# Kernel tuning notes

Hardware: AMD Instinct MI355X
Metric: run time of the kernel (lower is better)

## Reference

```python
import jax, jax.numpy as jnp
import numpy as np

N_NODES = 50000
N_EDGES = 800000
X_DIM = 64
STATE_DIM = 64
IN_DIM = X_DIM + STATE_DIM
OUT_DIM = 64
N_HEADS = 4
HEAD_DIM = OUT_DIM // N_HEADS
NEG_SLOPE = 0.2


def setup_inputs() -> dict:
    key = jax.random.key(0)
    ks = jax.random.split(key, 7)
    x = jax.random.normal(ks[0], (N_NODES, X_DIM), dtype=jnp.float32)
    state = jax.random.normal(ks[1], (N_NODES, STATE_DIM), dtype=jnp.float32)
    edge_index = jax.random.randint(ks[2], (2, N_EDGES), 0, N_NODES, dtype=jnp.int64)
    edge_weight = jax.random.uniform(ks[3], (N_EDGES,), dtype=jnp.float32)
    # xavier-uniform-like scales
    w_scale = float(np.sqrt(2.0 / (IN_DIM + OUT_DIM)))
    a_scale = float(np.sqrt(2.0 / (N_HEADS + HEAD_DIM)))
    W = jax.random.normal(ks[4], (OUT_DIM, IN_DIM), dtype=jnp.float32) * w_scale
    attn_src = jax.random.normal(ks[5], (N_HEADS, HEAD_DIM), dtype=jnp.float32) * a_scale
    attn_dst = jax.random.normal(ks[6], (N_HEADS, HEAD_DIM), dtype=jnp.float32) * a_scale
    return {"x": x, "state": state, "edge_index": edge_index, "edge_weight": edge_weight,
            "W": W, "attn_src": attn_src, "attn_dst": attn_dst}


def reference(x, state, edge_index, edge_weight, W, attn_src, attn_dst):
    # edge_weight is ignored by design (pure attention behavior)
    del edge_weight
    N = x.shape[0]
    H, D = attn_src.shape
    # linear_in (no bias): [N, IN_DIM] @ [IN_DIM, OUT_DIM]
    h_flat = jnp.concatenate([x, state], axis=-1) @ W.T          # [N, OUT_DIM]
    h = h_flat.reshape(N, H, D)                                   # [N, H, D]
    src = edge_index[0]
    dst = edge_index[1]
    # per-node attention scores, then gather per-edge (same math as gathering h first)
    s_src = jnp.einsum('nhd,hd->nh', h, attn_src)                 # [N, H]
    s_dst = jnp.einsum('nhd,hd->nh', h, attn_dst)                 # [N, H]
    logits = s_src[src] + s_dst[dst]                              # [E, H]
    logits = jnp.where(logits >= 0, logits, NEG_SLOPE * logits)   # leaky_relu
    # segment softmax over incoming edges of each dst node (stable, two-pass)
    max_by_dst = jax.ops.segment_max(logits, dst, num_segments=N) # [N, H]
    exp_shifted = jnp.exp(logits - max_by_dst[dst])               # [E, H]
    denom = jax.ops.segment_sum(exp_shifted, dst, num_segments=N) # [N, H]
    alpha = exp_shifted / (denom[dst] + 1e-12)                    # [E, H]
    # weighted message aggregation
    msg = h[src] * alpha[:, :, None]                              # [E, H, D]
    out_flat = jax.ops.segment_sum(msg.reshape(msg.shape[0], H * D), dst, num_segments=N)
    out_flat = out_flat + h_flat                                  # residual (shapes always match)
    out_flat = jax.nn.elu(out_flat)                               # activation
    return out_flat
```

## Files before the change

### kernel.cpp

```cpp
#include <hip/hip_runtime.h>
#include <hip/hip_bf16.h>

#define N_NODES 50000
#define N_EDGES 800000
#define NBK 196
#define BCAP 40
#define CAP  4864

typedef __attribute__((ext_vector_type(8))) short bf16x8;
typedef __attribute__((ext_vector_type(4))) float f32x4;

__device__ __forceinline__ unsigned short f2bu(float f) {
    __hip_bfloat16 hb = __float2bfloat16(f);
    return *(unsigned short*)&hb;
}
__device__ __forceinline__ unsigned pk2(float a, float b) {
    return (unsigned)f2bu(a) | ((unsigned)f2bu(b) << 16);
}

__global__ void __launch_bounds__(256, 4)
k1_mfma(const float* __restrict__ x, const float* __restrict__ state,
        const float* __restrict__ W, const float* __restrict__ a_src,
        const float* __restrict__ a_dst,
        float* __restrict__ hf32, float* __restrict__ s_src4,
        float* __restrict__ s_dst4, int* __restrict__ gcur) {
    __shared__ unsigned short alds[64 * 136];
    __shared__ unsigned short wlds[64 * 136];
    int tid = threadIdx.x;
    int nb = blockIdx.x * 64;

    if (blockIdx.x == 0 && tid < NBK) gcur[tid] = 0;

    const float4* x4  = (const float4*)x;
    const float4* st4 = (const float4*)state;
    const float4* W4  = (const float4*)W;
    for (int idx = tid; idx < 2048; idx += 256) {
        int row = idx >> 5, qc = idx & 31;
        int n = nb + row;
        float4 v = make_float4(0.f, 0.f, 0.f, 0.f);
        if (n < N_NODES)
            v = (qc < 16) ? x4[(long)n * 16 + qc] : st4[(long)n * 16 + (qc - 16)];
        unsigned* ap = (unsigned*)&alds[row * 136 + qc * 4];
        ap[0] = pk2(v.x, v.y);
        ap[1] = pk2(v.z, v.w);
        float4 wv = W4[idx];
        unsigned* wp = (unsigned*)&wlds[row * 136 + qc * 4];
        wp[0] = pk2(wv.x, wv.y);
        wp[1] = pk2(wv.z, wv.w);
    }
    __syncthreads();

    int lane = tid & 63;
    int w = tid >> 6;
    int lrow = lane & 15, lq = lane >> 4;

    f32x4 acc[4];
#pragma unroll
    for (int c = 0; c < 4; ++c) acc[c] = (f32x4){0.f, 0.f, 0.f, 0.f};

#pragma unroll
    for (int kc = 0; kc < 4; ++kc) {
        bf16x8 af = *(const bf16x8*)&alds[(w * 16 + lrow) * 136 + kc * 32 + lq * 8];
#pragma unroll
        for (int c = 0; c < 4; ++c) {
            bf16x8 bf = *(const bf16x8*)&wlds[(c * 16 + lrow) * 136 + kc * 32 + lq * 8];
            acc[c] = __builtin_amdgcn_mfma_f32_16x16x32_bf16(af, bf, acc[c], 0, 0, 0);
        }
    }
    __syncthreads();

    float* hst = (float*)alds;
#pragma unroll
    for (int r = 0; r < 4; ++r) {
        int nl = w * 16 + lq * 4 + r;
#pragma unroll
        for (int c = 0; c < 4; ++c)
            hst[nl * 68 + c * 16 + lrow] = acc[c][r];
    }
    __syncthreads();

    int node = tid >> 2, chunk = tid & 3;
    int n = nb + node;
    if (n < N_NODES) {
        const float* hp = &hst[node * 68 + chunk * 16];
        float hv[16];
        float vs = 0.f, vd = 0.f;
#pragma unroll
        for (int i = 0; i < 16; ++i) {
            hv[i] = hp[i];
            vs = fmaf(hv[i], a_src[chunk * 16 + i], vs);
            vd = fmaf(hv[i], a_dst[chunk * 16 + i], vd);
        }
        float* dst = hf32 + (long)n * 64 + chunk * 16;
        *(float4*)(dst + 0)  = make_float4(hv[0],  hv[1],  hv[2],  hv[3]);
        *(float4*)(dst + 4)  = make_float4(hv[4],  hv[5],  hv[6],  hv[7]);
        *(float4*)(dst + 8)  = make_float4(hv[8],  hv[9],  hv[10], hv[11]);
        *(float4*)(dst + 12) = make_float4(hv[12], hv[13], hv[14], hv[15]);
        s_src4[(long)nb * 4 + tid] = vs;
        s_dst4[(long)nb * 4 + tid] = vd;
    }
}

__global__ void __launch_bounds__(256)
k_bin(const int* __restrict__ ei, int* __restrict__ gcur, int* __restrict__ recs) {
    __shared__ int cnt[NBK];
    __shared__ int stage[NBK][BCAP];
    int tid = threadIdx.x;
    for (int i = tid; i < NBK; i += 256) cnt[i] = 0;
    __syncthreads();
    int e0 = blockIdx.x * 4096;
#pragma unroll
    for (int k = 0; k < 4; ++k) {
        int e = e0 + k * 1024 + tid * 4;
        if (e < N_EDGES) {
            int4 sv = *(const int4*)(ei + e);
            int4 dv = *(const int4*)(ei + N_EDGES + e);
            int ss[4] = {sv.x, sv.y, sv.z, sv.w};
            int dd[4] = {dv.x, dv.y, dv.z, dv.w};
#pragma unroll
            for (int j = 0; j < 4; ++j) {
                int b = dd[j] >> 8;
                int rec = ss[j] | ((dd[j] & 255) << 16);
                int p = atomicAdd(&cnt[b], 1);
                if (p < BCAP) stage[b][p] = rec;
                else {
                    int g = atomicAdd(&gcur[b], 1);
                    recs[b * CAP + g] = rec;
                }
            }
        }
    }
    __syncthreads();
    for (int b = tid; b < NBK; b += 256) {
        int nb = min(cnt[b], BCAP);
        if (nb > 0) {
            int g = atomicAdd(&gcur[b], nb);
            int d0 = b * CAP + g;
            for (int i = 0; i < nb; ++i) recs[d0 + i] = stage[b][i];
        }
    }
}

__global__ void __launch_bounds__(256)
k_sort(const int* __restrict__ recs, const int* __restrict__ gcur,
       int* __restrict__ recs2, int* __restrict__ off, int* __restrict__ deg) {
    __shared__ int cnt[256];
    __shared__ int pos[256];
    __shared__ int wsum[4];
    int tid = threadIdx.x, b = blockIdx.x;
    cnt[tid] = 0;
    __syncthreads();
    int base = b * CAP, cntb = gcur[b];
    for (int i = tid; i < cntb; i += 256)
        atomicAdd(&cnt[(recs[base + i] >> 16) & 255], 1);
    __syncthreads();
    int lane = tid & 63, wid = tid >> 6;
    int v = cnt[tid], inc = v;
#pragma unroll
    for (int s = 1; s < 64; s <<= 1) {
        int t = __shfl_up(inc, s);
        if (lane >= s) inc += t;
    }
    if (lane == 63) wsum[wid] = inc;
    __syncthreads();
    if (tid == 0) {
        int s = 0;
#pragma unroll
        for (int w = 0; w < 4; ++w) { int t = wsum[w]; wsum[w] = s; s += t; }
    }
    __syncthreads();
    int excl = wsum[wid] + inc - v;
    pos[tid] = excl;
    int n = b * 256 + tid;
    if (n < N_NODES) { off[n] = base + excl; deg[n] = v; }
    __syncthreads();
    for (int i = tid; i < cntb; i += 256) {
        int r = recs[base + i];
        int p = atomicAdd(&pos[(r >> 16) & 255], 1);
        recs2[base + p] = r & 0xFFFF;
    }
}

__global__ void k_agg(const int* __restrict__ off, const int* __restrict__ deg,
                      const int* __restrict__ csr, const float* __restrict__ s_src4,
                      const float* __restrict__ s_dst4,
                      const float* __restrict__ hf32, float* __restrict__ out) {
    int wave = threadIdx.x >> 6, lane = threadIdx.x & 63;
    int n = blockIdx.x * 4 + wave;
    if (n >= N_NODES) return;
    int q = lane >> 3, d = lane & 7, hh = d >> 1;
    int b = off[n], nE = deg[n];
    float sdh = s_dst4[(long)n * 4 + hh];

    float den = 0.f;
    float a0 = 0, a1 = 0, a2 = 0, a3 = 0, a4 = 0, a5 = 0, a6 = 0, a7 = 0;
    for (int c = 0; c < nE; c += 64) {
        int jn = min(64, nE - c);
        int svl = (lane < jn) ? csr[b + c + lane] : 0;
        for (int j = 0; j < jn; j += 16) {
            int j0 = j + q, j1 = j + 8 + q;
            float m0 = (j0 < jn) ? 1.f : 0.f;
            float m1 = (j1 < jn) ? 1.f : 0.f;
            int s0 = __shfl(svl, j0);
            int s1 = __shfl(svl, j1);
            float l0 = s_src4[s0 * 4 + hh];
            float l1 = s_src4[s1 * 4 + hh];
            const float4* p0 = (const float4*)(hf32 + (long)s0 * 64 + 8 * d);
            const float4* p1 = (const float4*)(hf32 + (long)s1 * 64 + 8 * d);
            float4 A0 = p0[0], A1 = p0[1];
            float4 B0 = p1[0], B1 = p1[1];
            l0 += sdh; l1 += sdh;
            float e0 = m0 * __expf(fmaxf(l0, 0.2f * l0));
            float e1 = m1 * __expf(fmaxf(l1, 0.2f * l1));
            den += e0 + e1;
            a0 = fmaf(e0, A0.x, a0); a1 = fmaf(e0, A0.y, a1);
            a2 = fmaf(e0, A0.z, a2); a3 = fmaf(e0, A0.w, a3);
            a4 = fmaf(e0, A1.x, a4); a5 = fmaf(e0, A1.y, a5);
            a6 = fmaf(e0, A1.z, a6); a7 = fmaf(e0, A1.w, a7);
            a0 = fmaf(e1, B0.x, a0); a1 = fmaf(e1, B0.y, a1);
            a2 = fmaf(e1, B0.z, a2); a3 = fmaf(e1, B0.w, a3);
            a4 = fmaf(e1, B1.x, a4); a5 = fmaf(e1, B1.y, a5);
            a6 = fmaf(e1, B1.z, a6); a7 = fmaf(e1, B1.w, a7);
        }
    }
#pragma unroll
    for (int o2 = 8; o2 < 64; o2 <<= 1) {
        den += __shfl_xor(den, o2);
        a0 += __shfl_xor(a0, o2);
        a1 += __shfl_xor(a1, o2);
        a2 += __shfl_xor(a2, o2);
        a3 += __shfl_xor(a3, o2);
        a4 += __shfl_xor(a4, o2);
        a5 += __shfl_xor(a5, o2);
        a6 += __shfl_xor(a6, o2);
        a7 += __shfl_xor(a7, o2);
    }

    if (q == 0) {
        const float4* hrp = (const float4*)(hf32 + (long)n * 64 + 8 * d);
        float4 r0 = hrp[0], r1 = hrp[1];
        float inv = 1.0f / (den + 1e-12f);
        float o0 = a0 * inv + r0.x, o1 = a1 * inv + r0.y;
        float o2 = a2 * inv + r0.z, o3 = a3 * inv + r0.w;
        float o4 = a4 * inv + r1.x, o5 = a5 * inv + r1.y;
        float o6 = a6 * inv + r1.z, o7 = a7 * inv + r1.w;
        o0 = (o0 > 0.f) ? o0 : __expf(o0) - 1.f;
        o1 = (o1 > 0.f) ? o1 : __expf(o1) - 1.f;
        o2 = (o2 > 0.f) ? o2 : __expf(o2) - 1.f;
        o3 = (o3 > 0.f) ? o3 : __expf(o3) - 1.f;
        o4 = (o4 > 0.f) ? o4 : __expf(o4) - 1.f;
        o5 = (o5 > 0.f) ? o5 : __expf(o5) - 1.f;
        o6 = (o6 > 0.f) ? o6 : __expf(o6) - 1.f;
        o7 = (o7 > 0.f) ? o7 : __expf(o7) - 1.f;
        float* op = &out[(long)n * 64 + 8 * d];
        *(float4*)(op + 0) = make_float4(o0, o1, o2, o3);
        *(float4*)(op + 4) = make_float4(o4, o5, o6, o7);
    }
}

extern "C" void kernel_launch(void* const* d_in, const int* in_sizes, int n_in,
                              void* d_out, int out_size, void* d_ws, size_t ws_size,
                              hipStream_t stream) {
    const float* x      = (const float*)d_in[0];
    const float* state  = (const float*)d_in[1];
    const int*   ei     = (const int*)d_in[2];
    const float* W      = (const float*)d_in[4];
    const float* a_src  = (const float*)d_in[5];
    const float* a_dst  = (const float*)d_in[6];

    float* out = (float*)d_out;

    float* hf32   = (float*)d_ws;
    float* s_src4 = hf32 + (long)N_NODES * 64;
    float* s_dst4 = s_src4 + (long)N_NODES * 4;
    int*   gcur   = (int*)(s_dst4 + (long)N_NODES * 4);
    int*   off    = gcur + 256;
    int*   deg    = off + N_NODES;
    int*   recs   = deg + N_NODES;
    int*   recs2  = recs + (long)NBK * CAP;

    k1_mfma<<<782, 256, 0, stream>>>(x, state, W, a_src, a_dst,
                                     hf32, s_src4, s_dst4, gcur);
    k_bin<<<196, 256, 0, stream>>>(ei, gcur, recs);
    k_sort<<<NBK, 256, 0, stream>>>(recs, gcur, recs2, off, deg);
    k_agg<<<(N_NODES + 3) / 4, 256, 0, stream>>>(off, deg, recs2, s_src4, s_dst4, hf32, out);
}
```

Baseline: 73.22 us.

## Store node features in bf16 and double rows per block in projection kernel

The projection kernel now writes h as packed bf16 instead of fp32, and the aggregation kernel gathers and unpacks bf16 rows, which halves the bytes moved per edge gather and for the residual. The projection kernel also processes 128 nodes per block, with two MFMA row tiles per wave, and launches half as many blocks. This reduces gather memory traffic at the cost of bf16 rounding in both the message values and the residual term.

```diff
diff --git a/kernel.cpp b/kernel.cpp
--- a/kernel.cpp
+++ b/kernel.cpp
@@ -10,6 +10,8 @@
 typedef __attribute__((ext_vector_type(8))) short bf16x8;
 typedef __attribute__((ext_vector_type(4))) float f32x4;
 
+__device__ __forceinline__ float blo(unsigned u) { return __uint_as_float(u << 16); }
+__device__ __forceinline__ float bhi(unsigned u) { return __uint_as_float(u & 0xffff0000u); }
 __device__ __forceinline__ unsigned short f2bu(float f) {
     __hip_bfloat16 hb = __float2bfloat16(f);
     return *(unsigned short*)&hb;
@@ -18,23 +20,23 @@
     return (unsigned)f2bu(a) | ((unsigned)f2bu(b) << 16);
 }
 
-__global__ void __launch_bounds__(256, 4)
+__global__ void __launch_bounds__(256, 3)
 k1_mfma(const float* __restrict__ x, const float* __restrict__ state,
         const float* __restrict__ W, const float* __restrict__ a_src,
         const float* __restrict__ a_dst,
-        float* __restrict__ hf32, float* __restrict__ s_src4,
+        unsigned short* __restrict__ hf2, float* __restrict__ s_src4,
         float* __restrict__ s_dst4, int* __restrict__ gcur) {
-    __shared__ unsigned short alds[64 * 136];
+    __shared__ unsigned short alds[128 * 136];
     __shared__ unsigned short wlds[64 * 136];
     int tid = threadIdx.x;
-    int nb = blockIdx.x * 64;
+    int nb = blockIdx.x * 128;
 
     if (blockIdx.x == 0 && tid < NBK) gcur[tid] = 0;
 
     const float4* x4  = (const float4*)x;
     const float4* st4 = (const float4*)state;
     const float4* W4  = (const float4*)W;
-    for (int idx = tid; idx < 2048; idx += 256) {
+    for (int idx = tid; idx < 4096; idx += 256) {
         int row = idx >> 5, qc = idx & 31;
         int n = nb + row;
         float4 v = make_float4(0.f, 0.f, 0.f, 0.f);
@@ -43,6 +45,9 @@
         unsigned* ap = (unsigned*)&alds[row * 136 + qc * 4];
         ap[0] = pk2(v.x, v.y);
         ap[1] = pk2(v.z, v.w);
+    }
+    for (int idx = tid; idx < 2048; idx += 256) {
+        int row = idx >> 5, qc = idx & 31;
         float4 wv = W4[idx];
         unsigned* wp = (unsigned*)&wlds[row * 136 + qc * 4];
         wp[0] = pk2(wv.x, wv.y);
@@ -54,50 +59,60 @@
     int w = tid >> 6;
     int lrow = lane & 15, lq = lane >> 4;
 
-    f32x4 acc[4];
-#pragma unroll
-    for (int c = 0; c < 4; ++c) acc[c] = (f32x4){0.f, 0.f, 0.f, 0.f};
+    f32x4 acc[2][4];
+#pragma unroll
+    for (int rt = 0; rt < 2; ++rt)
+#pragma unroll
+        for (int c = 0; c < 4; ++c) acc[rt][c] = (f32x4){0.f, 0.f, 0.f, 0.f};
 
 #pragma unroll
     for (int kc = 0; kc < 4; ++kc) {
-        bf16x8 af = *(const bf16x8*)&alds[(w * 16 + lrow) * 136 + kc * 32 + lq * 8];
+        bf16x8 af0 = *(const bf16x8*)&alds[(w * 32 + lrow) * 136 + kc * 32 + lq * 8];
+        bf16x8 af1 = *(const bf16x8*)&alds[(w * 32 + 16 + lrow) * 136 + kc * 32 + lq * 8];
 #pragma unroll
         for (int c = 0; c < 4; ++c) {
             bf16x8 bf = *(const bf16x8*)&wlds[(c * 16 + lrow) * 136 + kc * 32 + lq * 8];
-            acc[c] = __builtin_amdgcn_mfma_f32_16x16x32_bf16(af, bf, acc[c], 0, 0, 0);
+            acc[0][c] = __builtin_amdgcn_mfma_f32_16x16x32_bf16(af0, bf, acc[0][c], 0, 0, 0);
+            acc[1][c] = __builtin_amdgcn_mfma_f32_16x16x32_bf16(af1, bf, acc[1][c], 0, 0, 0);
         }
     }
     __syncthreads();
 
     float* hst = (float*)alds;
 #pragma unroll
-    for (int r = 0; r < 4; ++r) {
-        int nl = w * 16 + lq * 4 + r;
-#pragma unroll
-        for (int c = 0; c < 4; ++c)
-            hst[nl * 68 + c * 16 + lrow] = acc[c][r];
-    }
-    __syncthreads();
-
-    int node = tid >> 2, chunk = tid & 3;
-    int n = nb + node;
-    if (n < N_NODES) {
-        const float* hp = &hst[node * 68 + chunk * 16];
-        float hv[16];
-        float vs = 0.f, vd = 0.f;
-#pragma unroll
-        for (int i = 0; i < 16; ++i) {
-            hv[i] = hp[i];
-            vs = fmaf(hv[i], a_src[chunk * 16 + i], vs);
-            vd = fmaf(hv[i], a_dst[chunk * 16 + i], vd);
-        }
-        float* dst = hf32 + (long)n * 64 + chunk * 16;
-        *(float4*)(dst + 0)  = make_float4(hv[0],  hv[1],  hv[2],  hv[3]);
-        *(float4*)(dst + 4)  = make_float4(hv[4],  hv[5],  hv[6],  hv[7]);
-        *(float4*)(dst + 8)  = make_float4(hv[8],  hv[9],  hv[10], hv[11]);
-        *(float4*)(dst + 12) = make_float4(hv[12], hv[13], hv[14], hv[15]);
-        s_src4[(long)nb * 4 + tid] = vs;
-        s_dst4[(long)nb * 4 + tid] = vd;
+    for (int rt = 0; rt < 2; ++rt)
+#pragma unroll
+        for (int r = 0; r < 4; ++r) {
+            int nl = w * 32 + rt * 16 + lq * 4 + r;
+#pragma unroll
+            for (int c = 0; c < 4; ++c)
+                hst[nl * 68 + c * 16 + lrow] = acc[rt][c][r];
+        }
+    __syncthreads();
+
+#pragma unroll
+    for (int g = 0; g < 2; ++g) {
+        int node = (tid >> 2) + g * 64, chunk = tid & 3;
+        int n = nb + node;
+        if (n < N_NODES) {
+            const float* hp = &hst[node * 68 + chunk * 16];
+            float hv[16];
+            float vs = 0.f, vd = 0.f;
+#pragma unroll
+            for (int i = 0; i < 16; ++i) {
+                hv[i] = hp[i];
+                vs = fmaf(hv[i], a_src[chunk * 16 + i], vs);
+                vd = fmaf(hv[i], a_dst[chunk * 16 + i], vd);
+            }
+            unsigned pk[8];
+#pragma unroll
+            for (int j = 0; j < 8; ++j) pk[j] = pk2(hv[2 * j], hv[2 * j + 1]);
+            uint4* dst = (uint4*)(hf2 + (long)n * 64 + chunk * 16);
+            dst[0] = make_uint4(pk[0], pk[1], pk[2], pk[3]);
+            dst[1] = make_uint4(pk[4], pk[5], pk[6], pk[7]);
+            s_src4[(long)n * 4 + chunk] = vs;
+            s_dst4[(long)n * 4 + chunk] = vd;
+        }
     }
 }
 
@@ -184,7 +199,7 @@
 __global__ void k_agg(const int* __restrict__ off, const int* __restrict__ deg,
                       const int* __restrict__ csr, const float* __restrict__ s_src4,
                       const float* __restrict__ s_dst4,
-                      const float* __restrict__ hf32, float* __restrict__ out) {
+                      const unsigned short* __restrict__ h2, float* __restrict__ out) {
     int wave = threadIdx.x >> 6, lane = threadIdx.x & 63;
     int n = blockIdx.x * 4 + wave;
     if (n >= N_NODES) return;
@@ -205,22 +220,20 @@
             int s1 = __shfl(svl, j1);
             float l0 = s_src4[s0 * 4 + hh];
             float l1 = s_src4[s1 * 4 + hh];
-            const float4* p0 = (const float4*)(hf32 + (long)s0 * 64 + 8 * d);
-            const float4* p1 = (const float4*)(hf32 + (long)s1 * 64 + 8 * d);
-            float4 A0 = p0[0], A1 = p0[1];
-            float4 B0 = p1[0], B1 = p1[1];
+            uint4 A = *(const uint4*)(h2 + (long)s0 * 64 + 8 * d);
+            uint4 B = *(const uint4*)(h2 + (long)s1 * 64 + 8 * d);
             l0 += sdh; l1 += sdh;
             float e0 = m0 * __expf(fmaxf(l0, 0.2f * l0));
             float e1 = m1 * __expf(fmaxf(l1, 0.2f * l1));
             den += e0 + e1;
-            a0 = fmaf(e0, A0.x, a0); a1 = fmaf(e0, A0.y, a1);
-            a2 = fmaf(e0, A0.z, a2); a3 = fmaf(e0, A0.w, a3);
-            a4 = fmaf(e0, A1.x, a4); a5 = fmaf(e0, A1.y, a5);
-            a6 = fmaf(e0, A1.z, a6); a7 = fmaf(e0, A1.w, a7);
-            a0 = fmaf(e1, B0.x, a0); a1 = fmaf(e1, B0.y, a1);
-            a2 = fmaf(e1, B0.z, a2); a3 = fmaf(e1, B0.w, a3);
-            a4 = fmaf(e1, B1.x, a4); a5 = fmaf(e1, B1.y, a5);
-            a6 = fmaf(e1, B1.z, a6); a7 = fmaf(e1, B1.w, a7);
+            a0 = fmaf(e0, blo(A.x), a0); a1 = fmaf(e0, bhi(A.x), a1);
+            a2 = fmaf(e0, blo(A.y), a2); a3 = fmaf(e0, bhi(A.y), a3);
+            a4 = fmaf(e0, blo(A.z), a4); a5 = fmaf(e0, bhi(A.z), a5);
+            a6 = fmaf(e0, blo(A.w), a6); a7 = fmaf(e0, bhi(A.w), a7);
+            a0 = fmaf(e1, blo(B.x), a0); a1 = fmaf(e1, bhi(B.x), a1);
+            a2 = fmaf(e1, blo(B.y), a2); a3 = fmaf(e1, bhi(B.y), a3);
+            a4 = fmaf(e1, blo(B.z), a4); a5 = fmaf(e1, bhi(B.z), a5);
+            a6 = fmaf(e1, blo(B.w), a6); a7 = fmaf(e1, bhi(B.w), a7);
         }
     }
 #pragma unroll
@@ -237,13 +250,12 @@
     }
 
     if (q == 0) {
-        const float4* hrp = (const float4*)(hf32 + (long)n * 64 + 8 * d);
-        float4 r0 = hrp[0], r1 = hrp[1];
+        uint4 hr = *(const uint4*)(h2 + (long)n * 64 + 8 * d);
         float inv = 1.0f / (den + 1e-12f);
-        float o0 = a0 * inv + r0.x, o1 = a1 * inv + r0.y;
-        float o2 = a2 * inv + r0.z, o3 = a3 * inv + r0.w;
-        float o4 = a4 * inv + r1.x, o5 = a5 * inv + r1.y;
-        float o6 = a6 * inv + r1.z, o7 = a7 * inv + r1.w;
+        float o0 = a0 * inv + blo(hr.x), o1 = a1 * inv + bhi(hr.x);
+        float o2 = a2 * inv + blo(hr.y), o3 = a3 * inv + bhi(hr.y);
+        float o4 = a4 * inv + blo(hr.z), o5 = a5 * inv + bhi(hr.z);
+        float o6 = a6 * inv + blo(hr.w), o7 = a7 * inv + bhi(hr.w);
         o0 = (o0 > 0.f) ? o0 : __expf(o0) - 1.f;
         o1 = (o1 > 0.f) ? o1 : __expf(o1) - 1.f;
         o2 = (o2 > 0.f) ? o2 : __expf(o2) - 1.f;
@@ -270,8 +282,8 @@
 
     float* out = (float*)d_out;
 
-    float* hf32   = (float*)d_ws;
-    float* s_src4 = hf32 + (long)N_NODES * 64;
+    unsigned short* hf2 = (unsigned short*)d_ws;
+    float* s_src4 = (float*)(hf2 + (long)N_NODES * 64);
     float* s_dst4 = s_src4 + (long)N_NODES * 4;
     int*   gcur   = (int*)(s_dst4 + (long)N_NODES * 4);
     int*   off    = gcur + 256;
@@ -279,9 +291,9 @@
     int*   recs   = deg + N_NODES;
     int*   recs2  = recs + (long)NBK * CAP;
 
-    k1_mfma<<<782, 256, 0, stream>>>(x, state, W, a_src, a_dst,
-                                     hf32, s_src4, s_dst4, gcur);
+    k1_mfma<<<391, 256, 0, stream>>>(x, state, W, a_src, a_dst,
+                                     hf2, s_src4, s_dst4, gcur);
     k_bin<<<196, 256, 0, stream>>>(ei, gcur, recs);
     k_sort<<<NBK, 256, 0, stream>>>(recs, gcur, recs2, off, deg);
-    k_agg<<<(N_NODES + 3) / 4, 256, 0, stream>>>(off, deg, recs2, s_src4, s_dst4, hf32, out);
-}
+    k_agg<<<(N_NODES + 3) / 4, 256, 0, stream>>>(off, deg, recs2, s_src4, s_dst4, hf2, out);
+}
```

Measured after the change: 66.02 us. 9.8% less time.
